# Kernel tuning notes

Measured on AMD Instinct MI355X. Metric: run time of the kernel, lower is better.

## Reference

```python
import jax, jax.numpy as jnp
import numpy as np

B, NPG = 64, 512          # graphs, nodes per graph
N_TOTAL = B * NPG
LIG = 128                 # ligand nodes per graph (segment 0); rest are protein (segment 1)
BOX = 40.0                # Angstrom box for random coords -> realistic radius-graph density
INTER_CUTOFF = 10.0       # normalize_coord is identity (scale=1)
INTRA_CUTOFF = 8.0


def setup_inputs() -> dict:
    key = jax.random.key(0)
    X = jax.random.uniform(key, (N_TOTAL, 1, 3), dtype=jnp.float32) * BOX
    batch_id = jnp.repeat(jnp.arange(B, dtype=jnp.int32), NPG)
    local = jnp.tile(jnp.arange(NPG, dtype=jnp.int32), B)
    segment_id = (local >= LIG).astype(jnp.int32)
    is_global = jnp.logical_or(local == 0, local == LIG)  # one global node per segment
    return {"X": X, "batch_id": batch_id, "segment_id": segment_id, "is_global": is_global}


def _radial_edges(X, src_dst, cutoff):
    # src_dst: [E, 2] node indices; X: [N, C, 3], channel 0 holds coords
    p = X[:, 0][src_dst]                              # [E, 2, 3]
    dist = jnp.linalg.norm(p[:, 0] - p[:, 1], axis=-1)
    return src_dst[dist <= cutoff].T                  # [2, E']


def reference(X, batch_id, segment_id, is_global):
    N = batch_id.shape[0]
    nB = int(batch_id[-1]) + 1
    lengths = jax.ops.segment_sum(jnp.ones_like(batch_id), batch_id, num_segments=nB)
    max_n = int(jnp.max(lengths))
    offsets = jnp.concatenate([jnp.zeros((1,), lengths.dtype), jnp.cumsum(lengths)[:-1]])
    gni = jnp.arange(N)
    gni2lni = gni - offsets[batch_id]                 # local node index within its graph

    # Dense [N, max_n] same-batch mask via cumsum trick (O(N*max_n))
    same_bid = jnp.zeros((N, max_n), jnp.float32)
    same_bid = same_bid.at[gni, lengths[batch_id] - 1].set(1.0)
    same_bid = 1.0 - jnp.cumsum(same_bid, axis=-1)
    same_bid = jnp.concatenate([jnp.ones((N, 1), jnp.float32), same_bid[:, :-1]], axis=-1)
    same_bid = same_bid.at[gni, gni2lni].set(0.0)     # remove self edges

    row, col = jnp.nonzero(same_bid)                  # all same-graph candidate pairs
    col = col + offsets[batch_id[row]]                # local col -> global node index

    row_global = is_global[row]
    col_global = is_global[col]
    not_global = jnp.logical_not(jnp.logical_or(row_global, col_global))
    row_seg = segment_id[row]
    col_seg = segment_id[col]

    # intra-protein context edges (segment 1, within 8A)
    sel = (row_seg == col_seg) & (row_seg == 1) & not_global
    ctx_edges = _radial_edges(X, jnp.stack([row[sel], col[sel]], axis=1), INTRA_CUTOFF)

    # inter ligand-protein edges (within 10A)
    sel = (row_seg != col_seg) & not_global
    ir, ic = row[sel], col[sel]
    inter_edges = _radial_edges(X, jnp.stack([ir, ic], axis=1), INTER_CUTOFF)
    if inter_edges.shape[1] == 0:
        inter_edges = jnp.array([[ir[0], ic[0]], [ic[0], ir[0]]], dtype=inter_edges.dtype)

    reduced_inter_edge_batchid = batch_id[inter_edges[0][inter_edges[0] < inter_edges[1]]]
    reduced_inter_edge_offsets = offsets[reduced_inter_edge_batchid]

    # global<->same-segment edges and global<->global edges appended to context
    sel = (row_seg == col_seg) & jnp.logical_not(not_global)
    global_normal = jnp.stack([row[sel], col[sel]])
    sel = row_global & col_global
    global_global = jnp.stack([row[sel], col[sel]])
    ctx_edges = jnp.concatenate([ctx_edges, global_normal, global_global], axis=1)

    return ctx_edges, inter_edges, reduced_inter_edge_batchid, reduced_inter_edge_offsets
```

## Files before the change

kernel.cpp:

```cpp
#include <hip/hip_runtime.h>

#define N_TOTAL 32768
#define NB 64
#define NPG 512
#define LIG 128
#define NBLK 256
#define ROWS_PER_BLK 128

__device__ __forceinline__ bool dist_ok(float dx, float dy, float dz, float cutoff) {
    float s = __fadd_rn(__fadd_rn(__fmul_rn(dx, dx), __fmul_rn(dy, dy)), __fmul_rn(dz, dz));
    return __fsqrt_rn(s) <= cutoff;
}

__global__ __launch_bounds__(1024) void count_kernel(const float* __restrict__ X,
                                                     int* __restrict__ ctx_cnt,
                                                     int* __restrict__ inter_cnt,
                                                     int* __restrict__ bp) {
    __shared__ float s[NPG * 3];
    __shared__ int swc[16], swi[16];
    const int b = blockIdx.x;
    const int g = b >> 2;
    const int q = b & 3;
    const int t = threadIdx.x;
    if (t < 384) ((float4*)s)[t] = ((const float4*)X)[g * 384 + t];
    __syncthreads();
    const int lane = t & 63;
    const int w = t >> 6;
    int wc = 0, wi = 0;
    for (int j = 0; j < 8; ++j) {
        const int r = q * 128 + w * 8 + j;
        const float px = s[3 * r], py = s[3 * r + 1], pz = s[3 * r + 2];
        int cctx = 0, cint = 0;
        if (q == 0) {
            if (r != 0) {
                for (int k = 2; k < 8; ++k) {
                    const int c = k * 64 + lane;
                    const bool pred = (c > LIG) &&
                        dist_ok(px - s[3 * c], py - s[3 * c + 1], pz - s[3 * c + 2], 10.0f);
                    cint += __popcll(__ballot(pred));
                }
            }
        } else {
            if (r != LIG) {
                for (int k = 0; k < 2; ++k) {
                    const int c = k * 64 + lane;
                    const bool pred = (c >= 1) && (c < LIG) &&
                        dist_ok(px - s[3 * c], py - s[3 * c + 1], pz - s[3 * c + 2], 10.0f);
                    cint += __popcll(__ballot(pred));
                }
                for (int k = 2; k < 8; ++k) {
                    const int c = k * 64 + lane;
                    const bool pred = (c > LIG) && (c != r) &&
                        dist_ok(px - s[3 * c], py - s[3 * c + 1], pz - s[3 * c + 2], 8.0f);
                    cctx += __popcll(__ballot(pred));
                }
            }
        }
        if (lane == 0) {
            const int row = g * NPG + r;
            ctx_cnt[row] = cctx;
            inter_cnt[row] = cint;
        }
        wc += cctx; wi += cint;
    }
    if (lane == 0) { swc[w] = wc; swi[w] = wi; }
    __syncthreads();
    if (t == 0) {
        int sc_ = 0, si_ = 0;
        for (int k = 0; k < 16; ++k) { sc_ += swc[k]; si_ += swi[k]; }
        bp[b] = sc_;
        bp[NBLK + b] = si_;
        bp[2 * NBLK + b] = (q == 0) ? si_ : 0;
    }
}

__global__ __launch_bounds__(NBLK) void midscan_kernel(const int* __restrict__ bp,
                                                       int* __restrict__ bb,
                                                       int* __restrict__ totals) {
    __shared__ int s0[NBLK], s1[NBLK], s2[NBLK];
    const int t = threadIdx.x;
    const int c = bp[t], i = bp[NBLK + t], r = bp[2 * NBLK + t];
    s0[t] = c; s1[t] = i; s2[t] = r;
    __syncthreads();
    for (int off = 1; off < NBLK; off <<= 1) {
        int v0 = 0, v1 = 0, v2 = 0;
        if (t >= off) { v0 = s0[t - off]; v1 = s1[t - off]; v2 = s2[t - off]; }
        __syncthreads();
        s0[t] += v0; s1[t] += v1; s2[t] += v2;
        __syncthreads();
    }
    bb[t] = s0[t] - c;
    bb[NBLK + t] = s1[t] - i;
    bb[2 * NBLK + t] = s2[t] - r;
    if (t == NBLK - 1) { totals[0] = s0[t]; totals[1] = s1[t]; totals[2] = s2[t]; }
}

__global__ __launch_bounds__(1024) void emit_kernel(const float* __restrict__ X,
                                                    const int* __restrict__ ctx_cnt,
                                                    const int* __restrict__ inter_cnt,
                                                    const int* __restrict__ bb,
                                                    const int* __restrict__ totals,
                                                    int* __restrict__ out) {
    __shared__ float s[NPG * 3];
    __shared__ int sc[ROWS_PER_BLK], si[ROWS_PER_BLK], sr[ROWS_PER_BLK];
    const int b = blockIdx.x;
    const int g = b >> 2;
    const int q = b & 3;
    const int t = threadIdx.x;
    if (t < 384) ((float4*)s)[t] = ((const float4*)X)[g * 384 + t];
    int mc = 0, mi = 0, mr = 0;
    const int row0 = g * NPG + q * 128;
    if (t < 128) {
        mc = ctx_cnt[row0 + t];
        mi = inter_cnt[row0 + t];
        mr = (q == 0 && t >= 1) ? mi : 0;
        sc[t] = mc; si[t] = mi; sr[t] = mr;
    }
    __syncthreads();
    for (int off = 1; off < 128; off <<= 1) {
        int v0 = 0, v1 = 0, v2 = 0;
        if (t >= off && t < 128) { v0 = sc[t - off]; v1 = si[t - off]; v2 = sr[t - off]; }
        __syncthreads();
        if (t < 128) { sc[t] += v0; si[t] += v1; sr[t] += v2; }
        __syncthreads();
    }
    if (t < 128) {
        sc[t] += bb[b] - mc;
        si[t] += bb[NBLK + b] - mi;
        sr[t] += bb[2 * NBLK + b] - mr;
    }
    __syncthreads();

    const int lane = t & 63;
    const int w = t >> 6;
    const unsigned long long lmask = (1ull << lane) - 1ull;
    const int gn = g * NPG;

    const int Eci = totals[0];
    const int Ei  = totals[1];
    const int Er  = totals[2];
    const int Ectx = Eci + NB * 1020 + NB * 2;

    int* ctx_src   = out;
    int* ctx_dst   = out + Ectx;
    int* inter_src = out + 2 * Ectx;
    int* inter_dst = inter_src + Ei;
    int* red_bid   = out + 2 * Ectx + 2 * Ei;
    int* red_off   = red_bid + Er;

    for (int j = 0; j < 8; ++j) {
        const int lr = w * 8 + j;
        const int r = q * 128 + lr;
        const int row = gn + r;
        const float px = s[3 * r], py = s[3 * r + 1], pz = s[3 * r + 2];

        if (q == 0) {
            if (r == 0) {
                for (int k = 0; k < 2; ++k) {
                    const int c = k * 64 + lane;
                    if (c >= 1 && c < LIG) {
                        const int pos = Eci + g * 1020 + (c - 1);
                        ctx_src[pos] = row; ctx_dst[pos] = gn + c;
                    }
                }
                if (lane == 0) {
                    const int pos = Eci + NB * 1020 + g * 2;
                    ctx_src[pos] = row; ctx_dst[pos] = gn + LIG;
                }
            } else {
                int ib = si[lr];
                int rb = sr[lr];
                for (int k = 2; k < 8; ++k) {
                    const int c = k * 64 + lane;
                    const bool pred = (c > LIG) &&
                        dist_ok(px - s[3 * c], py - s[3 * c + 1], pz - s[3 * c + 2], 10.0f);
                    const unsigned long long m = __ballot(pred);
                    if (pred) {
                        const int p = __popcll(m & lmask);
                        inter_src[ib + p] = row; inter_dst[ib + p] = gn + c;
                        red_bid[rb + p] = g;     red_off[rb + p] = gn;
                    }
                    const int cnt = __popcll(m);
                    ib += cnt; rb += cnt;
                }
                if (lane == 0) {
                    const int pos = Eci + g * 1020 + (LIG - 1) + (r - 1);
                    ctx_src[pos] = row; ctx_dst[pos] = gn;
                }
            }
        } else {
            if (r == LIG) {
                for (int k = 2; k < 8; ++k) {
                    const int c = k * 64 + lane;
                    if (c > LIG) {
                        const int pos = Eci + g * 1020 + 2 * (LIG - 1) + (c - LIG - 1);
                        ctx_src[pos] = row; ctx_dst[pos] = gn + c;
                    }
                }
                if (lane == 0) {
                    const int pos = Eci + NB * 1020 + g * 2 + 1;
                    ctx_src[pos] = row; ctx_dst[pos] = gn;
                }
            } else {
                int ib = si[lr];
                for (int k = 0; k < 2; ++k) {
                    const int c = k * 64 + lane;
                    const bool pred = (c >= 1) && (c < LIG) &&
                        dist_ok(px - s[3 * c], py - s[3 * c + 1], pz - s[3 * c + 2], 10.0f);
                    const unsigned long long m = __ballot(pred);
                    if (pred) {
                        const int pos = ib + __popcll(m & lmask);
                        inter_src[pos] = row; inter_dst[pos] = gn + c;
                    }
                    ib += __popcll(m);
                }
                int cb = sc[lr];
                for (int k = 2; k < 8; ++k) {
                    const int c = k * 64 + lane;
                    const bool pred = (c > LIG) && (c != r) &&
                        dist_ok(px - s[3 * c], py - s[3 * c + 1], pz - s[3 * c + 2], 8.0f);
                    const unsigned long long m = __ballot(pred);
                    if (pred) {
                        const int pos = cb + __popcll(m & lmask);
                        ctx_src[pos] = row; ctx_dst[pos] = gn + c;
                    }
                    cb += __popcll(m);
                }
                if (lane == 0) {
                    const int pos = Eci + g * 1020 + 2 * (LIG - 1) + (NPG - LIG - 1) + (r - LIG - 1);
                    ctx_src[pos] = row; ctx_dst[pos] = gn + LIG;
                }
            }
        }
    }
}

extern "C" void kernel_launch(void* const* d_in, const int* in_sizes, int n_in,
                              void* d_out, int out_size, void* d_ws, size_t ws_size,
                              hipStream_t stream) {
    (void)in_sizes; (void)n_in; (void)out_size; (void)ws_size;
    const float* X = (const float*)d_in[0];
    int* ws = (int*)d_ws;
    int* ctx_cnt   = ws;
    int* inter_cnt = ws + N_TOTAL;
    int* bp        = ws + 2 * N_TOTAL;
    int* bb        = bp + 3 * NBLK;
    int* totals    = bb + 3 * NBLK;
    int* out       = (int*)d_out;

    count_kernel<<<NBLK, 1024, 0, stream>>>(X, ctx_cnt, inter_cnt, bp);
    midscan_kernel<<<1, NBLK, 0, stream>>>(bp, bb, totals);
    emit_kernel<<<NBLK, 1024, 0, stream>>>(X, ctx_cnt, inter_cnt, bb, totals, out);
}
```

Before: 92.59 us.

## Fuse count, scan and emit into one cooperative kernel with cached ballot masks

Replaces the three-kernel pipeline (count, single-block midscan, emit) with one cooperative kernel that uses a grid-wide sync between the per-block count/scan and the emit phase. Each block keeps its ballot masks in shared memory so the distance tests are not recomputed during emit. Every block redundantly scans the 256 block partials after the grid sync. This removes two kernel launches, the global round-trip of per-row counts, and the duplicated distance math, at the cost of cooperative-launch constraints (all 256 blocks of 1024 threads must be co-resident) and a grid barrier.

```diff
diff --git a/kernel.cpp b/kernel.cpp
--- a/kernel.cpp
+++ b/kernel.cpp
@@ -1,4 +1,7 @@
 #include <hip/hip_runtime.h>
+#include <hip/hip_cooperative_groups.h>
+
+namespace cg = cooperative_groups;
 
 #define N_TOTAL 32768
 #define NB 64
@@ -12,23 +15,31 @@
     return __fsqrt_rn(s) <= cutoff;
 }
 
-__global__ __launch_bounds__(1024) void count_kernel(const float* __restrict__ X,
-                                                     int* __restrict__ ctx_cnt,
-                                                     int* __restrict__ inter_cnt,
-                                                     int* __restrict__ bp) {
+__global__ __launch_bounds__(1024) void fused_kernel(const float* __restrict__ X,
+                                                     int* __restrict__ bp,
+                                                     int* __restrict__ out) {
     __shared__ float s[NPG * 3];
-    __shared__ int swc[16], swi[16];
+    __shared__ unsigned long long smask[ROWS_PER_BLK * 8];
+    __shared__ int rc[ROWS_PER_BLK], ri[ROWS_PER_BLK];
+    __shared__ int sc[ROWS_PER_BLK], si[ROWS_PER_BLK], sr[ROWS_PER_BLK];
+    __shared__ int s0[NBLK], s1[NBLK], s2[NBLK];
+    __shared__ int blkb[3], tot[3];
+
     const int b = blockIdx.x;
     const int g = b >> 2;
     const int q = b & 3;
     const int t = threadIdx.x;
-    if (t < 384) ((float4*)s)[t] = ((const float4*)X)[g * 384 + t];
-    __syncthreads();
     const int lane = t & 63;
     const int w = t >> 6;
-    int wc = 0, wi = 0;
+    const unsigned long long lmask = (1ull << lane) - 1ull;
+    const int gn = g * NPG;
+
+    if (t < 384) ((float4*)s)[t] = ((const float4*)X)[g * 384 + t];
+    __syncthreads();
+
     for (int j = 0; j < 8; ++j) {
-        const int r = q * 128 + w * 8 + j;
+        const int lr = w * 8 + j;
+        const int r = q * 128 + lr;
         const float px = s[3 * r], py = s[3 * r + 1], pz = s[3 * r + 2];
         int cctx = 0, cint = 0;
         if (q == 0) {
@@ -37,85 +48,39 @@
                     const int c = k * 64 + lane;
                     const bool pred = (c > LIG) &&
                         dist_ok(px - s[3 * c], py - s[3 * c + 1], pz - s[3 * c + 2], 10.0f);
-                    cint += __popcll(__ballot(pred));
+                    const unsigned long long m = __ballot(pred);
+                    if (lane == 0) smask[lr * 8 + k] = m;
+                    cint += __popcll(m);
                 }
             }
         } else {
-            if (r != LIG) {
+            if (lr != 0) {
+            }
+            if (!(q == 1 && lr == 0)) {
+                const int r_ = r;
                 for (int k = 0; k < 2; ++k) {
                     const int c = k * 64 + lane;
                     const bool pred = (c >= 1) && (c < LIG) &&
                         dist_ok(px - s[3 * c], py - s[3 * c + 1], pz - s[3 * c + 2], 10.0f);
-                    cint += __popcll(__ballot(pred));
-                }
-                for (int k = 2; k < 8; ++k) {
-                    const int c = k * 64 + lane;
-                    const bool pred = (c > LIG) && (c != r) &&
+                    const unsigned long long m = __ballot(pred);
+                    if (lane == 0) smask[lr * 8 + k] = m;
+                    cint += __popcll(m);
+                }
+                for (int k = 2; k < 8; ++k) {
+                    const int c = k * 64 + lane;
+                    const bool pred = (c > LIG) && (c != r_) &&
                         dist_ok(px - s[3 * c], py - s[3 * c + 1], pz - s[3 * c + 2], 8.0f);
-                    cctx += __popcll(__ballot(pred));
+                    const unsigned long long m = __ballot(pred);
+                    if (lane == 0) smask[lr * 8 + k] = m;
+                    cctx += __popcll(m);
                 }
             }
         }
-        if (lane == 0) {
-            const int row = g * NPG + r;
-            ctx_cnt[row] = cctx;
-            inter_cnt[row] = cint;
-        }
-        wc += cctx; wi += cint;
-    }
-    if (lane == 0) { swc[w] = wc; swi[w] = wi; }
-    __syncthreads();
-    if (t == 0) {
-        int sc_ = 0, si_ = 0;
-        for (int k = 0; k < 16; ++k) { sc_ += swc[k]; si_ += swi[k]; }
-        bp[b] = sc_;
-        bp[NBLK + b] = si_;
-        bp[2 * NBLK + b] = (q == 0) ? si_ : 0;
-    }
-}
-
-__global__ __launch_bounds__(NBLK) void midscan_kernel(const int* __restrict__ bp,
-                                                       int* __restrict__ bb,
-                                                       int* __restrict__ totals) {
-    __shared__ int s0[NBLK], s1[NBLK], s2[NBLK];
-    const int t = threadIdx.x;
-    const int c = bp[t], i = bp[NBLK + t], r = bp[2 * NBLK + t];
-    s0[t] = c; s1[t] = i; s2[t] = r;
-    __syncthreads();
-    for (int off = 1; off < NBLK; off <<= 1) {
-        int v0 = 0, v1 = 0, v2 = 0;
-        if (t >= off) { v0 = s0[t - off]; v1 = s1[t - off]; v2 = s2[t - off]; }
-        __syncthreads();
-        s0[t] += v0; s1[t] += v1; s2[t] += v2;
-        __syncthreads();
-    }
-    bb[t] = s0[t] - c;
-    bb[NBLK + t] = s1[t] - i;
-    bb[2 * NBLK + t] = s2[t] - r;
-    if (t == NBLK - 1) { totals[0] = s0[t]; totals[1] = s1[t]; totals[2] = s2[t]; }
-}
-
-__global__ __launch_bounds__(1024) void emit_kernel(const float* __restrict__ X,
-                                                    const int* __restrict__ ctx_cnt,
-                                                    const int* __restrict__ inter_cnt,
-                                                    const int* __restrict__ bb,
-                                                    const int* __restrict__ totals,
-                                                    int* __restrict__ out) {
-    __shared__ float s[NPG * 3];
-    __shared__ int sc[ROWS_PER_BLK], si[ROWS_PER_BLK], sr[ROWS_PER_BLK];
-    const int b = blockIdx.x;
-    const int g = b >> 2;
-    const int q = b & 3;
-    const int t = threadIdx.x;
-    if (t < 384) ((float4*)s)[t] = ((const float4*)X)[g * 384 + t];
-    int mc = 0, mi = 0, mr = 0;
-    const int row0 = g * NPG + q * 128;
-    if (t < 128) {
-        mc = ctx_cnt[row0 + t];
-        mi = inter_cnt[row0 + t];
-        mr = (q == 0 && t >= 1) ? mi : 0;
-        sc[t] = mc; si[t] = mi; sr[t] = mr;
-    }
+        if (lane == 0) { rc[lr] = cctx; ri[lr] = cint; }
+    }
+    __syncthreads();
+
+    if (t < 128) { sc[t] = rc[t]; si[t] = ri[t]; sr[t] = (q == 0) ? ri[t] : 0; }
     __syncthreads();
     for (int off = 1; off < 128; off <<= 1) {
         int v0 = 0, v1 = 0, v2 = 0;
@@ -124,21 +89,44 @@
         if (t < 128) { sc[t] += v0; si[t] += v1; sr[t] += v2; }
         __syncthreads();
     }
+    if (t == 127) {
+        bp[b] = sc[127];
+        bp[NBLK + b] = si[127];
+        bp[2 * NBLK + b] = sr[127];
+        __threadfence();
+    }
+
+    cg::this_grid().sync();
+
+    const int tt = t & 255;
+    const int arr = t >> 8;
+    int mine = 0;
+    int* sp = (arr == 0) ? s0 : (arr == 1) ? s1 : s2;
+    if (arr < 3) { mine = bp[arr * NBLK + tt]; sp[tt] = mine; }
+    __syncthreads();
+    for (int off = 1; off < NBLK; off <<= 1) {
+        int v = 0;
+        if (arr < 3 && tt >= off) v = sp[tt - off];
+        __syncthreads();
+        if (arr < 3 && tt >= off) sp[tt] += v;
+        __syncthreads();
+    }
+    if (arr < 3) {
+        if (tt == b) blkb[arr] = sp[tt] - mine;
+        if (tt == NBLK - 1) tot[arr] = sp[NBLK - 1];
+    }
+    __syncthreads();
+
     if (t < 128) {
-        sc[t] += bb[b] - mc;
-        si[t] += bb[NBLK + b] - mi;
-        sr[t] += bb[2 * NBLK + b] - mr;
-    }
-    __syncthreads();
-
-    const int lane = t & 63;
-    const int w = t >> 6;
-    const unsigned long long lmask = (1ull << lane) - 1ull;
-    const int gn = g * NPG;
-
-    const int Eci = totals[0];
-    const int Ei  = totals[1];
-    const int Er  = totals[2];
+        sc[t] += blkb[0] - rc[t];
+        si[t] += blkb[1] - ri[t];
+        sr[t] += blkb[2] - ((q == 0) ? ri[t] : 0);
+    }
+    __syncthreads();
+
+    const int Eci = tot[0];
+    const int Ei  = tot[1];
+    const int Er  = tot[2];
     const int Ectx = Eci + NB * 1020 + NB * 2;
 
     int* ctx_src   = out;
@@ -152,7 +140,6 @@
         const int lr = w * 8 + j;
         const int r = q * 128 + lr;
         const int row = gn + r;
-        const float px = s[3 * r], py = s[3 * r + 1], pz = s[3 * r + 2];
 
         if (q == 0) {
             if (r == 0) {
@@ -171,11 +158,9 @@
                 int ib = si[lr];
                 int rb = sr[lr];
                 for (int k = 2; k < 8; ++k) {
-                    const int c = k * 64 + lane;
-                    const bool pred = (c > LIG) &&
-                        dist_ok(px - s[3 * c], py - s[3 * c + 1], pz - s[3 * c + 2], 10.0f);
-                    const unsigned long long m = __ballot(pred);
-                    if (pred) {
+                    const unsigned long long m = smask[lr * 8 + k];
+                    if ((m >> lane) & 1ull) {
+                        const int c = k * 64 + lane;
                         const int p = __popcll(m & lmask);
                         inter_src[ib + p] = row; inter_dst[ib + p] = gn + c;
                         red_bid[rb + p] = g;     red_off[rb + p] = gn;
@@ -189,7 +174,7 @@
                 }
             }
         } else {
-            if (r == LIG) {
+            if (q == 1 && lr == 0) {
                 for (int k = 2; k < 8; ++k) {
                     const int c = k * 64 + lane;
                     if (c > LIG) {
@@ -204,11 +189,9 @@
             } else {
                 int ib = si[lr];
                 for (int k = 0; k < 2; ++k) {
-                    const int c = k * 64 + lane;
-                    const bool pred = (c >= 1) && (c < LIG) &&
-                        dist_ok(px - s[3 * c], py - s[3 * c + 1], pz - s[3 * c + 2], 10.0f);
-                    const unsigned long long m = __ballot(pred);
-                    if (pred) {
+                    const unsigned long long m = smask[lr * 8 + k];
+                    if ((m >> lane) & 1ull) {
+                        const int c = k * 64 + lane;
                         const int pos = ib + __popcll(m & lmask);
                         inter_src[pos] = row; inter_dst[pos] = gn + c;
                     }
@@ -216,11 +199,9 @@
                 }
                 int cb = sc[lr];
                 for (int k = 2; k < 8; ++k) {
-                    const int c = k * 64 + lane;
-                    const bool pred = (c > LIG) && (c != r) &&
-                        dist_ok(px - s[3 * c], py - s[3 * c + 1], pz - s[3 * c + 2], 8.0f);
-                    const unsigned long long m = __ballot(pred);
-                    if (pred) {
+                    const unsigned long long m = smask[lr * 8 + k];
+                    if ((m >> lane) & 1ull) {
+                        const int c = k * 64 + lane;
                         const int pos = cb + __popcll(m & lmask);
                         ctx_src[pos] = row; ctx_dst[pos] = gn + c;
                     }
@@ -240,15 +221,9 @@
                               hipStream_t stream) {
     (void)in_sizes; (void)n_in; (void)out_size; (void)ws_size;
     const float* X = (const float*)d_in[0];
-    int* ws = (int*)d_ws;
-    int* ctx_cnt   = ws;
-    int* inter_cnt = ws + N_TOTAL;
-    int* bp        = ws + 2 * N_TOTAL;
-    int* bb        = bp + 3 * NBLK;
-    int* totals    = bb + 3 * NBLK;
-    int* out       = (int*)d_out;
-
-    count_kernel<<<NBLK, 1024, 0, stream>>>(X, ctx_cnt, inter_cnt, bp);
-    midscan_kernel<<<1, NBLK, 0, stream>>>(bp, bb, totals);
-    emit_kernel<<<NBLK, 1024, 0, stream>>>(X, ctx_cnt, inter_cnt, bb, totals, out);
+    int* bp = (int*)d_ws;
+    int* out = (int*)d_out;
+
+    void* args[] = {(void*)&X, (void*)&bp, (void*)&out};
+    hipLaunchCooperativeKernel((void*)fused_kernel, dim3(NBLK), dim3(1024), args, 0, stream);
 }
```

After: 145.2 us. +56.8%, slower.
